# Optimization experiments

Hardware: AMD Instinct MI355X
Metric: run time of the kernel (lower is better)

## Reference

```python
import jax, jax.numpy as jnp
import numpy as np

FEATURE_DIM = 2048
CROP_PE_DIM = 96
FULL = FEATURE_DIM + CROP_PE_DIM  # 2144
H1 = 1024
H2 = 512
NEG_SLOPE = 0.01


def leaky(x):
    return jnp.where(x >= 0, x, NEG_SLOPE * x)


def setup_inputs() -> dict:
    key = jax.random.key(0)
    ks = jax.random.split(key, 8)
    B, T = 512, 32
    features = jax.random.normal(ks[0], (B, T, FULL), dtype=jnp.float32)

    def lin(k, fan_in, fan_out):
        kw, kb = jax.random.split(k)
        bound = 1.0 / np.sqrt(fan_in)
        W = jax.random.uniform(kw, (fan_in, fan_out), minval=-bound, maxval=bound, dtype=jnp.float32)
        b = jax.random.uniform(kb, (fan_out,), minval=-bound, maxval=bound, dtype=jnp.float32)
        return W, b

    We, be = lin(ks[1], 2 * FULL, H1)
    W1a, b1a = lin(ks[2], H1, H1)
    W1b, b1b = lin(ks[3], H1, H2)
    W2a, b2a = lin(ks[4], H2, H2)
    W2b, b2b = lin(ks[5], H2, H2)
    Wd, bd = lin(ks[6], H2, 3)
    return {
        "features": features,
        "We": We, "be": be,
        "W1a": W1a, "b1a": b1a, "W1b": W1b, "b1b": b1b,
        "W2a": W2a, "b2a": b2a, "W2b": W2b, "b2b": b2b,
        "Wd": Wd, "bd": bd,
    }


def reference(features, We, be, W1a, b1a, W1b, b1b, W2a, b2a, W2b, b2b, Wd, bd):
    B, T, D = features.shape
    # Vectorized version of the double Python loop: pair each token with token 0.
    anchor = jnp.broadcast_to(features[:, :1, :], (B, T, D))  # features[i][0]
    features_full = jnp.concatenate((features, anchor), axis=-1).reshape(B * T, 2 * D)
    e_f = features_full @ We + be
    h = leaky(leaky(e_f) @ W1a + b1a)
    h = h @ W1b + b1b  # block1 output
    h2 = leaky(leaky(h) @ W2a + b2a) @ W2b + b2b  # block2
    h = h + h2
    translations = leaky(h) @ Wd + bd  # (B*T, 3)
    bias = jnp.array([[0.0, 0.0, 1.0]], dtype=translations.dtype)
    return translations + bias
```

## Files before the change

### kernel.cpp

```cpp
#include <hip/hip_runtime.h>
#include <hip/hip_bf16.h>
#include <stdint.h>

typedef __attribute__((ext_vector_type(4))) float f32x4;
typedef __attribute__((ext_vector_type(8))) short bf16x8;

#define BK 64

__device__ inline void gload_lds16(const void* g, void* l) {
    __builtin_amdgcn_global_load_lds(
        (const __attribute__((address_space(1))) void*)g,
        (__attribute__((address_space(3))) void*)l, 16, 0, 0);
}

__device__ inline void wg_barrier() {
    asm volatile("s_barrier" ::: "memory");
}
#define SCHED0 __builtin_amdgcn_sched_barrier(0)
#define VMW(n) asm volatile("s_waitcnt vmcnt(" #n ")" ::: "memory")

__device__ inline int xcd_swizzle(int orig, int nwg) {
    int q = nwg >> 3, r = nwg & 7;
    int xcd = orig & 7, idx = orig >> 3;
    int base = (xcd < r) ? xcd * (q + 1) : r * (q + 1) + (xcd - r) * q;
    return base + idx;
}

__device__ inline float b2f(short s) {
    union { float f; unsigned u; } x; x.u = ((unsigned)(unsigned short)s) << 16; return x.f;
}
__device__ inline short f2bs(float f) {
    __hip_bfloat16 h = __float2bfloat16(f);
    short s; __builtin_memcpy(&s, &h, 2); return s;
}

__device__ inline void wt_tile(const float* __restrict__ W, __hip_bfloat16* __restrict__ WT,
                               int K, int N, int KP, int tid, int bid) {
    __shared__ float tile[32][33];
    const int ntn = N >> 5;
    const int tk = bid / ntn, tn = bid - tk * ntn;
    const int k0 = tk * 32, n0 = tn * 32;
    const int c = tid & 31, r8 = tid >> 5;
    #pragma unroll
    for (int p = 0; p < 4; p++) {
        int k = k0 + r8 + p * 8;
        tile[r8 + p * 8][c] = (k < K) ? W[(size_t)k * N + n0 + c] : 0.f;
    }
    __syncthreads();
    #pragma unroll
    for (int p = 0; p < 4; p++) {
        int n = n0 + r8 + p * 8;
        WT[(size_t)n * KP + k0 + c] = __float2bfloat16(tile[c][r8 + p * 8]);
    }
}

__global__ __launch_bounds__(256)
void prepass(const float* __restrict__ feat, __hip_bfloat16* __restrict__ featbf,
             const float* __restrict__ We, __hip_bfloat16* __restrict__ WeTt,
             __hip_bfloat16* __restrict__ WeTb,
             const float* __restrict__ W1a, __hip_bfloat16* __restrict__ W1aT,
             const float* __restrict__ W1b, __hip_bfloat16* __restrict__ W1bT,
             const float* __restrict__ W2a, __hip_bfloat16* __restrict__ W2aT,
             const float* __restrict__ W2b, __hip_bfloat16* __restrict__ W2bT)
{
    const int bid = blockIdx.x;
    const int tid = threadIdx.x;
    if (bid < 17408) {
        int i = bid * 256 + tid;
        int r = i / 272, c8 = (i % 272) * 8;
        __hip_bfloat16 tmp[8];
        if (c8 < 2144) {
            const float4* p = (const float4*)(feat + (size_t)r * 2144 + c8);
            float4 x0 = p[0], x1 = p[1];
            tmp[0] = __float2bfloat16(x0.x); tmp[1] = __float2bfloat16(x0.y);
            tmp[2] = __float2bfloat16(x0.z); tmp[3] = __float2bfloat16(x0.w);
            tmp[4] = __float2bfloat16(x1.x); tmp[5] = __float2bfloat16(x1.y);
            tmp[6] = __float2bfloat16(x1.z); tmp[7] = __float2bfloat16(x1.w);
        } else {
            #pragma unroll
            for (int j = 0; j < 8; j++) tmp[j] = __float2bfloat16(0.f);
        }
        *(bf16x8*)&featbf[(size_t)r * 2176 + c8] = *(const bf16x8*)tmp;
        return;
    }
    int b = bid - 17408;
    if      (b < 2176) wt_tile(We,                WeTt, 2144, 1024, 2176, tid, b);
    else if (b < 4352) wt_tile(We + 2144 * 1024,  WeTb, 2144, 1024, 2176, tid, b - 2176);
    else if (b < 5376) wt_tile(W1a, W1aT, 1024, 1024, 1024, tid, b - 4352);
    else if (b < 5888) wt_tile(W1b, W1bT, 1024,  512, 1024, tid, b - 5376);
    else if (b < 6144) wt_tile(W2a, W2aT,  512,  512,  512, tid, b - 5888);
    else               wt_tile(W2b, W2bT,  512,  512,  512, tid, b - 6144);
}

template<int BN_, int RES_MODE, int OUTK>
__global__ __launch_bounds__(512, 2)
void gemmk(const __hip_bfloat16* __restrict__ A, int lda,
           const __hip_bfloat16* __restrict__ Bt,
           const float* __restrict__ bias,
           const __hip_bfloat16* __restrict__ resb,
           const float* __restrict__ resf,
           __hip_bfloat16* __restrict__ outb,
           __hip_bfloat16* __restrict__ outb2,
           float* __restrict__ outf,
           int M, int N, int K, int gx)
{
    constexpr int NF  = BN_ / 64;
    constexpr int REL = NF * 16;
    __shared__ __hip_bfloat16 lds[2][(256 + BN_) * BK];

    const int nwg  = gridDim.x;
    const int wgid = xcd_swizzle(blockIdx.x, nwg);
    const int by   = wgid / gx;
    const int bx   = wgid - by * gx;

    const int t    = threadIdx.x;
    const int lane = t & 63;
    const int wv   = t >> 6;
    const int wr   = wv >> 2;
    const int wc   = wv & 3;

    const int row0 = by * 256;
    const int col0 = bx * BN_;

    const int NT = K / BK;
    const int split = blockIdx.y;
    const int kb = (split * NT) / gridDim.y;
    const int ke = ((split + 1) * NT) / gridDim.y;
    float* outfs = outf;
    if (OUTK == 0 && gridDim.y > 1) outfs = outf + (size_t)split * M * N;

    const int srow = t >> 3;
    const int sc8  = (t & 7) * 8;
    const int scol = sc8 ^ ((srow & 7) << 3);
    const int sdst = sc8;

    f32x4 acc[8][NF];
    #pragma unroll
    for (int i = 0; i < 8; i++)
        #pragma unroll
        for (int j = 0; j < NF; j++)
            acc[i][j] = f32x4{0.f, 0.f, 0.f, 0.f};

    const int lrow = lane & 15;
    const int lk   = (lane >> 4) * 8;
    const int rxor = (lrow & 7) << 3;

    auto stA = [&](int buf, int k0, int b) {
        gload_lds16(A + (size_t)(row0 + b * 64 + srow) * lda + k0 + scol,
                    &lds[buf][(b * 64 + srow) * BK + sdst]);
    };
    auto stB = [&](int buf, int k0, int b) {
        gload_lds16(Bt + (size_t)(col0 + b * 64 + srow) * K + k0 + scol,
                    &lds[buf][(256 + b * 64 + srow) * BK + sdst]);
    };

    bf16x8 af[4][2];
    auto rdA = [&](int buf, int ih) {
        #pragma unroll
        for (int i = 0; i < 4; ++i)
            #pragma unroll
            for (int h = 0; h < 2; ++h)
                af[i][h] = *(const bf16x8*)
                    &lds[buf][(wr * 128 + (ih * 4 + i) * 16 + lrow) * BK + ((h * 32 + lk) ^ rxor)];
    };
    bf16x8 bgl[2][2], bgh[2][2];
    auto rdB2 = [&](int buf, int jb, bf16x8 (&bg)[2][2]) {
        #pragma unroll
        for (int j = 0; j < 2; ++j)
            #pragma unroll
            for (int h = 0; h < 2; ++h)
                bg[j][h] = *(const bf16x8*)
                    &lds[buf][(256 + wc * REL + (jb + j) * 16 + lrow) * BK + ((h * 32 + lk) ^ rxor)];
    };

#define MFMA_Q(BG, IB, JB)                                                    \
    do {                                                                      \
        __builtin_amdgcn_s_setprio(1);                                        \
        _Pragma("unroll") for (int h_ = 0; h_ < 2; ++h_)                      \
        _Pragma("unroll") for (int i_ = 0; i_ < 4; ++i_)                      \
        _Pragma("unroll") for (int j_ = 0; j_ < 2; ++j_)                      \
            acc[(IB) + i_][(JB) + j_] = __builtin_amdgcn_mfma_f32_16x16x32_bf16( \
                af[i_][h_], BG[j_][h_], acc[(IB) + i_][(JB) + j_], 0, 0, 0);  \
        __builtin_amdgcn_s_setprio(0);                                        \
    } while (0)

    {
        const int k0 = kb * BK, k1 = (kb + 1) * BK;
        if constexpr (NF == 4) {
            stA(0, k0, 0); stA(0, k0, 2); stA(0, k0, 1); stA(0, k0, 3);
            stB(0, k0, 0); stB(0, k0, 1); stB(0, k0, 2); stB(0, k0, 3);
            stA(1, k1, 0); stA(1, k1, 2); stA(1, k1, 1); stA(1, k1, 3);
        } else {
            stA(0, k0, 0); stA(0, k0, 2); stB(0, k0, 0); stB(0, k0, 1);
            stA(0, k0, 1); stA(0, k0, 3);
            stA(1, k1, 0); stA(1, k1, 2); stB(1, k1, 0); stB(1, k1, 1);
        }
    }

    int cur = 0;
    for (int kt = kb; kt < ke; ++kt) {
        const bool pf1 = (kt + 1 < ke), pf2 = (kt + 2 < ke);
        const int nk1 = (kt + 1) * BK, nk2 = (kt + 2) * BK;
        const int nxt = cur ^ 1;
        if constexpr (NF == 4) {
            if (kt == ke - 1) VMW(0); else VMW(4);
            wg_barrier();
            rdA(cur, 0); rdB2(cur, 0, bgl);
            if (pf1) { stB(nxt, nk1, 0); stB(nxt, nk1, 1); }
            SCHED0;
            MFMA_Q(bgl, 0, 0);
            wg_barrier();
            rdB2(cur, 2, bgh);
            if (pf1) { stB(nxt, nk1, 2); stB(nxt, nk1, 3); }
            SCHED0;
            MFMA_Q(bgh, 0, 2);
            wg_barrier();
            rdA(cur, 1);
            if (pf2) { stA(cur, nk2, 0); stA(cur, nk2, 2); }
            SCHED0;
            MFMA_Q(bgl, 4, 0);
            wg_barrier();
            if (pf2) { stA(cur, nk2, 1); stA(cur, nk2, 3); }
            SCHED0;
            MFMA_Q(bgh, 4, 2);
        } else {
            if (kt == ke - 1) VMW(2); else VMW(6);
            wg_barrier();
            rdA(cur, 0); rdB2(cur, 0, bgl);
            if (pf1) { stA(nxt, nk1, 1); stA(nxt, nk1, 3); }
            SCHED0;
            MFMA_Q(bgl, 0, 0);
            if (kt == ke - 1) VMW(0); else VMW(6);
            wg_barrier();
            rdA(cur, 1);
            if (pf2) { stA(cur, nk2, 0); stA(cur, nk2, 2); stB(cur, nk2, 0); stB(cur, nk2, 1); }
            SCHED0;
            MFMA_Q(bgl, 4, 0);
        }
        cur ^= 1;
    }
#undef MFMA_Q

    if constexpr (OUTK == 0) {
        #pragma unroll
        for (int j = 0; j < NF; j++) {
            const int col = col0 + wc * REL + j * 16 + lrow;
            #pragma unroll
            for (int i = 0; i < 8; i++) {
                const int rbase = row0 + wr * 128 + i * 16 + (lane >> 4) * 4;
                #pragma unroll
                for (int r = 0; r < 4; r++)
                    outfs[(size_t)(rbase + r) * N + col] = acc[i][j][r];
            }
        }
    } else {
        wg_barrier();
        __hip_bfloat16* eb = &lds[0][0] + wv * (128 * REL);
        #pragma unroll
        for (int i = 0; i < 8; i++)
            #pragma unroll
            for (int j = 0; j < NF; j++)
                #pragma unroll
                for (int r = 0; r < 4; r++)
                    eb[(i * 16 + (lane >> 4) * 4 + r) * REL + j * 16 + lrow] =
                        __float2bfloat16(acc[i][j][r]);
        constexpr int LPR = REL / 8;
        constexpr int RPI = 64 / LPR;
        constexpr int NIT = 128 / RPI;
        const int lrr = lane / LPR;
        const int lcc = (lane % LPR) * 8;
        const int col = col0 + wc * REL + lcc;
        float bvv[8];
        if (bias) {
            float4 b0 = *(const float4*)&bias[col];
            float4 b1 = *(const float4*)&bias[col + 4];
            bvv[0] = b0.x; bvv[1] = b0.y; bvv[2] = b0.z; bvv[3] = b0.w;
            bvv[4] = b1.x; bvv[5] = b1.y; bvv[6] = b1.z; bvv[7] = b1.w;
        } else {
            #pragma unroll
            for (int e = 0; e < 8; e++) bvv[e] = 0.f;
        }
        #pragma unroll
        for (int it = 0; it < NIT; it++) {
            const int rl  = it * RPI + lrr;
            const int row = row0 + wr * 128 + rl;
            bf16x8 v8 = *(bf16x8*)&eb[rl * REL + lcc];
            float vv[8];
            #pragma unroll
            for (int e = 0; e < 8; e++) vv[e] = b2f(v8[e]) + bvv[e];
            if constexpr (RES_MODE == 1) {
                bf16x8 r8 = *(const bf16x8*)&resb[(size_t)row * N + col];
                #pragma unroll
                for (int e = 0; e < 8; e++) vv[e] += b2f(r8[e]);
            }
            if constexpr (RES_MODE == 2) {
                const float* rp = &resf[(size_t)(row >> 5) * N + col];
                float4 r0 = *(const float4*)rp;
                float4 r1 = *(const float4*)(rp + 4);
                vv[0] += r0.x; vv[1] += r0.y; vv[2] += r0.z; vv[3] += r0.w;
                vv[4] += r1.x; vv[5] += r1.y; vv[6] += r1.z; vv[7] += r1.w;
            }
            bf16x8 o1, o2;
            #pragma unroll
            for (int e = 0; e < 8; e++) {
                float lv = vv[e] >= 0.f ? vv[e] : 0.01f * vv[e];
                if constexpr (OUTK == 1) o1[e] = f2bs(lv);
                if constexpr (OUTK == 2) o1[e] = f2bs(vv[e]);
                if constexpr (OUTK == 3) { o1[e] = f2bs(lv); o2[e] = f2bs(vv[e]); }
            }
            *(bf16x8*)&outb[(size_t)row * N + col] = o1;
            if constexpr (OUTK == 3)
                *(bf16x8*)&outb2[(size_t)row * N + col] = o2;
        }
    }
}

__global__ __launch_bounds__(256)
void anchor_reduce(const float* __restrict__ part, const float* __restrict__ be,
                   float* __restrict__ out) {
    int i = blockIdx.x * 256 + threadIdx.x;
    if (i >= 512 * 1024) return;
    const int S = 512 * 1024;
    int col = i & 1023;
    float s = be[col];
    #pragma unroll
    for (int p = 0; p < 16; p++) s += part[i + p * S];
    out[i] = s;
}

__global__ __launch_bounds__(256)
void final_head(const __hip_bfloat16* __restrict__ h, const float* __restrict__ Wd,
                const float* __restrict__ bd, float* __restrict__ out)
{
    int row  = blockIdx.x * 4 + (threadIdx.x >> 6);
    int lane = threadIdx.x & 63;
    const __hip_bfloat16* hr = h + (size_t)row * 512;
    bf16x8 v8 = *(const bf16x8*)&hr[lane * 8];
    float s0 = 0.f, s1 = 0.f, s2 = 0.f;
    #pragma unroll
    for (int e = 0; e < 8; e++) {
        float v = b2f(v8[e]);
        v = v >= 0.f ? v : 0.01f * v;
        int k = lane * 8 + e;
        s0 += v * Wd[k * 3 + 0];
        s1 += v * Wd[k * 3 + 1];
        s2 += v * Wd[k * 3 + 2];
    }
    #pragma unroll
    for (int off = 32; off > 0; off >>= 1) {
        s0 += __shfl_down(s0, off);
        s1 += __shfl_down(s1, off);
        s2 += __shfl_down(s2, off);
    }
    if (lane == 0) {
        out[row * 3 + 0] = s0 + bd[0];
        out[row * 3 + 1] = s1 + bd[1];
        out[row * 3 + 2] = s2 + bd[2] + 1.0f;
    }
}

extern "C" void kernel_launch(void* const* d_in, const int* in_sizes, int n_in,
                              void* d_out, int out_size, void* d_ws, size_t ws_size,
                              hipStream_t stream)
{
    const float* features = (const float*)d_in[0];
    const float* We  = (const float*)d_in[1];
    const float* be  = (const float*)d_in[2];
    const float* W1a = (const float*)d_in[3];
    const float* b1a = (const float*)d_in[4];
    const float* W1b = (const float*)d_in[5];
    const float* b1b = (const float*)d_in[6];
    const float* W2a = (const float*)d_in[7];
    const float* b2a = (const float*)d_in[8];
    const float* W2b = (const float*)d_in[9];
    const float* b2b = (const float*)d_in[10];
    const float* Wd  = (const float*)d_in[11];
    const float* bd  = (const float*)d_in[12];
    float* out = (float*)d_out;

    char* ws = (char*)d_ws;
    size_t off = 0;
    auto alloc = [&](size_t bytes) -> char* {
        char* p = ws + off;
        off += (bytes + 255) & ~(size_t)255;
        return p;
    };
    __hip_bfloat16* featbf = (__hip_bfloat16*)alloc(16384ull * 2176 * 2);
    __hip_bfloat16* WeTt   = (__hip_bfloat16*)alloc(1024ull * 2176 * 2);
    __hip_bfloat16* WeTb   = (__hip_bfloat16*)alloc(1024ull * 2176 * 2);
    __hip_bfloat16* W1aT   = (__hip_bfloat16*)alloc(1024ull * 1024 * 2);
    __hip_bfloat16* W1bT   = (__hip_bfloat16*)alloc(512ull * 1024 * 2);
    __hip_bfloat16* W2aT   = (__hip_bfloat16*)alloc(512ull * 512 * 2);
    __hip_bfloat16* W2bT   = (__hip_bfloat16*)alloc(512ull * 512 * 2);
    float* eanchor_part    = (float*)alloc(16ull * 512 * 1024 * 4);
    float* eanchor         = (float*)alloc(512ull * 1024 * 4);
    char* bufA             = alloc(16384ull * 1024 * 2);
    char* bufB             = alloc(16384ull * 1024 * 2);
    __hip_bfloat16* h1b    = (__hip_bfloat16*)alloc(16384ull * 512 * 2);

    __hip_bfloat16* act1   = (__hip_bfloat16*)bufA;
    __hip_bfloat16* act2   = (__hip_bfloat16*)bufB;
    __hip_bfloat16* act3   = (__hip_bfloat16*)bufA;
    __hip_bfloat16* act4   = (__hip_bfloat16*)bufB;
    __hip_bfloat16* hsum_b = (__hip_bfloat16*)bufA;

    prepass<<<17408 + 6400, 256, 0, stream>>>(
        features, featbf, We, WeTt, WeTb, W1a, W1aT, W1b, W1bT, W2a, W2aT, W2b, W2bT);

    gemmk<256, 0, 0><<<dim3(8, 16), 512, 0, stream>>>(
        featbf, 32 * 2176, WeTb, nullptr, nullptr, nullptr,
        nullptr, nullptr, eanchor_part, 512, 1024, 2176, 4);
    anchor_reduce<<<2048, 256, 0, stream>>>(eanchor_part, be, eanchor);

    gemmk<256, 2, 1><<<dim3(256), 512, 0, stream>>>(
        featbf, 2176, WeTt, nullptr, nullptr, eanchor,
        act1, nullptr, nullptr, 16384, 1024, 2176, 4);

    gemmk<256, 0, 1><<<dim3(256), 512, 0, stream>>>(
        act1, 1024, W1aT, b1a, nullptr, nullptr,
        act2, nullptr, nullptr, 16384, 1024, 1024, 4);

    gemmk<128, 0, 3><<<dim3(256), 512, 0, stream>>>(
        act2, 1024, W1bT, b1b, nullptr, nullptr,
        act3, h1b, nullptr, 16384, 512, 1024, 4);

    gemmk<128, 0, 1><<<dim3(256), 512, 0, stream>>>(
        act3, 512, W2aT, b2a, nullptr, nullptr,
        act4, nullptr, nullptr, 16384, 512, 512, 4);

    gemmk<128, 1, 2><<<dim3(256), 512, 0, stream>>>(
        act4, 512, W2bT, b2b, h1b, nullptr,
        hsum_b, nullptr, nullptr, 16384, 512, 512, 4);

    final_head<<<4096, 256, 0, stream>>>(hsum_b, Wd, bd, out);
}
```

Measured before the change: 229.6 us.

## Fuse final 512→3 head into last GEMM epilogue, halve anchor split-K

The last GEMM epilogue now applies the leaky activation and the 512x3 head projection in registers, reduces partial sums through shuffles and LDS, and writes per-column-tile partials. A tiny reduce kernel then adds the bias, which removes the bf16 hsum write and its re-read. The prepass feature cast now uses nontemporal loads and stores. The anchor split-K grid drops from 16 to 8 partitions, which means less partial traffic but less parallelism.

```diff
diff --git a/kernel.cpp b/kernel.cpp
--- a/kernel.cpp
+++ b/kernel.cpp
@@ -68,19 +68,18 @@
     if (bid < 17408) {
         int i = bid * 256 + tid;
         int r = i / 272, c8 = (i % 272) * 8;
-        __hip_bfloat16 tmp[8];
+        bf16x8 o;
         if (c8 < 2144) {
-            const float4* p = (const float4*)(feat + (size_t)r * 2144 + c8);
-            float4 x0 = p[0], x1 = p[1];
-            tmp[0] = __float2bfloat16(x0.x); tmp[1] = __float2bfloat16(x0.y);
-            tmp[2] = __float2bfloat16(x0.z); tmp[3] = __float2bfloat16(x0.w);
-            tmp[4] = __float2bfloat16(x1.x); tmp[5] = __float2bfloat16(x1.y);
-            tmp[6] = __float2bfloat16(x1.z); tmp[7] = __float2bfloat16(x1.w);
+            const f32x4* p = (const f32x4*)(feat + (size_t)r * 2144 + c8);
+            f32x4 x0 = __builtin_nontemporal_load(p);
+            f32x4 x1 = __builtin_nontemporal_load(p + 1);
+            o[0] = f2bs(x0[0]); o[1] = f2bs(x0[1]); o[2] = f2bs(x0[2]); o[3] = f2bs(x0[3]);
+            o[4] = f2bs(x1[0]); o[5] = f2bs(x1[1]); o[6] = f2bs(x1[2]); o[7] = f2bs(x1[3]);
         } else {
             #pragma unroll
-            for (int j = 0; j < 8; j++) tmp[j] = __float2bfloat16(0.f);
-        }
-        *(bf16x8*)&featbf[(size_t)r * 2176 + c8] = *(const bf16x8*)tmp;
+            for (int j = 0; j < 8; j++) o[j] = f2bs(0.f);
+        }
+        __builtin_nontemporal_store(o, (bf16x8*)&featbf[(size_t)r * 2176 + c8]);
         return;
     }
     int b = bid - 17408;
@@ -102,6 +101,8 @@
            __hip_bfloat16* __restrict__ outb,
            __hip_bfloat16* __restrict__ outb2,
            float* __restrict__ outf,
+           const float* __restrict__ Wd,
+           float* __restrict__ hpart,
            int M, int N, int K, int gx)
 {
     constexpr int NF  = BN_ / 64;
@@ -256,6 +257,7 @@
     } else {
         wg_barrier();
         __hip_bfloat16* eb = &lds[0][0] + wv * (128 * REL);
+        float* sp = (float*)(&lds[0][0] + 8 * 128 * REL);
         #pragma unroll
         for (int i = 0; i < 8; i++)
             #pragma unroll
@@ -300,17 +302,45 @@
                 vv[0] += r0.x; vv[1] += r0.y; vv[2] += r0.z; vv[3] += r0.w;
                 vv[4] += r1.x; vv[5] += r1.y; vv[6] += r1.z; vv[7] += r1.w;
             }
-            bf16x8 o1, o2;
-            #pragma unroll
-            for (int e = 0; e < 8; e++) {
-                float lv = vv[e] >= 0.f ? vv[e] : 0.01f * vv[e];
-                if constexpr (OUTK == 1) o1[e] = f2bs(lv);
-                if constexpr (OUTK == 2) o1[e] = f2bs(vv[e]);
-                if constexpr (OUTK == 3) { o1[e] = f2bs(lv); o2[e] = f2bs(vv[e]); }
+            if constexpr (OUTK == 4) {
+                float t0 = 0.f, t1 = 0.f, t2 = 0.f;
+                #pragma unroll
+                for (int e = 0; e < 8; e++) {
+                    float lv = vv[e] >= 0.f ? vv[e] : 0.01f * vv[e];
+                    const float* wd = &Wd[(size_t)(col + e) * 3];
+                    t0 += lv * wd[0]; t1 += lv * wd[1]; t2 += lv * wd[2];
+                }
+                t0 += __shfl_xor(t0, 1); t0 += __shfl_xor(t0, 2);
+                t1 += __shfl_xor(t1, 1); t1 += __shfl_xor(t1, 2);
+                t2 += __shfl_xor(t2, 1); t2 += __shfl_xor(t2, 2);
+                if ((lane & 3) == 0) {
+                    float* q = &sp[(size_t)(wr * 128 + rl) * 12 + wc * 3];
+                    q[0] = t0; q[1] = t1; q[2] = t2;
+                }
+            } else {
+                bf16x8 o1, o2;
+                #pragma unroll
+                for (int e = 0; e < 8; e++) {
+                    float lv = vv[e] >= 0.f ? vv[e] : 0.01f * vv[e];
+                    if constexpr (OUTK == 1) o1[e] = f2bs(lv);
+                    if constexpr (OUTK == 2) o1[e] = f2bs(vv[e]);
+                    if constexpr (OUTK == 3) { o1[e] = f2bs(lv); o2[e] = f2bs(vv[e]); }
+                }
+                *(bf16x8*)&outb[(size_t)row * N + col] = o1;
+                if constexpr (OUTK == 3)
+                    *(bf16x8*)&outb2[(size_t)row * N + col] = o2;
             }
-            *(bf16x8*)&outb[(size_t)row * N + col] = o1;
-            if constexpr (OUTK == 3)
-                *(bf16x8*)&outb2[(size_t)row * N + col] = o2;
+        }
+        if constexpr (OUTK == 4) {
+            wg_barrier();
+            if (t < 256) {
+                const float* q = &sp[(size_t)t * 12];
+                float a0 = q[0] + q[3] + q[6] + q[9];
+                float a1 = q[1] + q[4] + q[7] + q[10];
+                float a2 = q[2] + q[5] + q[8] + q[11];
+                float* hp = &hpart[(size_t)(row0 + t) * 12 + bx * 3];
+                hp[0] = a0; hp[1] = a1; hp[2] = a2;
+            }
         }
     }
 }
@@ -324,39 +354,20 @@
     int col = i & 1023;
     float s = be[col];
     #pragma unroll
-    for (int p = 0; p < 16; p++) s += part[i + p * S];
+    for (int p = 0; p < 8; p++) s += part[i + p * S];
     out[i] = s;
 }
 
 __global__ __launch_bounds__(256)
-void final_head(const __hip_bfloat16* __restrict__ h, const float* __restrict__ Wd,
-                const float* __restrict__ bd, float* __restrict__ out)
+void head_reduce(const float* __restrict__ hpart, const float* __restrict__ bd,
+                 float* __restrict__ out)
 {
-    int row  = blockIdx.x * 4 + (threadIdx.x >> 6);
-    int lane = threadIdx.x & 63;
-    const __hip_bfloat16* hr = h + (size_t)row * 512;
-    bf16x8 v8 = *(const bf16x8*)&hr[lane * 8];
-    float s0 = 0.f, s1 = 0.f, s2 = 0.f;
-    #pragma unroll
-    for (int e = 0; e < 8; e++) {
-        float v = b2f(v8[e]);
-        v = v >= 0.f ? v : 0.01f * v;
-        int k = lane * 8 + e;
-        s0 += v * Wd[k * 3 + 0];
-        s1 += v * Wd[k * 3 + 1];
-        s2 += v * Wd[k * 3 + 2];
-    }
-    #pragma unroll
-    for (int off = 32; off > 0; off >>= 1) {
-        s0 += __shfl_down(s0, off);
-        s1 += __shfl_down(s1, off);
-        s2 += __shfl_down(s2, off);
-    }
-    if (lane == 0) {
-        out[row * 3 + 0] = s0 + bd[0];
-        out[row * 3 + 1] = s1 + bd[1];
-        out[row * 3 + 2] = s2 + bd[2] + 1.0f;
-    }
+    int row = blockIdx.x * 256 + threadIdx.x;
+    if (row >= 16384) return;
+    const float* p = hpart + (size_t)row * 12;
+    out[row * 3 + 0] = p[0] + p[3] + p[6] + p[9]  + bd[0];
+    out[row * 3 + 1] = p[1] + p[4] + p[7] + p[10] + bd[1];
+    out[row * 3 + 2] = p[2] + p[5] + p[8] + p[11] + bd[2] + 1.0f;
 }
 
 extern "C" void kernel_launch(void* const* d_in, const int* in_sizes, int n_in,
@@ -392,45 +403,45 @@
     __hip_bfloat16* W1bT   = (__hip_bfloat16*)alloc(512ull * 1024 * 2);
     __hip_bfloat16* W2aT   = (__hip_bfloat16*)alloc(512ull * 512 * 2);
     __hip_bfloat16* W2bT   = (__hip_bfloat16*)alloc(512ull * 512 * 2);
-    float* eanchor_part    = (float*)alloc(16ull * 512 * 1024 * 4);
+    float* eanchor_part    = (float*)alloc(8ull * 512 * 1024 * 4);
     float* eanchor         = (float*)alloc(512ull * 1024 * 4);
     char* bufA             = alloc(16384ull * 1024 * 2);
     char* bufB             = alloc(16384ull * 1024 * 2);
     __hip_bfloat16* h1b    = (__hip_bfloat16*)alloc(16384ull * 512 * 2);
+    float* hpart           = (float*)alloc(16384ull * 12 * 4);
 
     __hip_bfloat16* act1   = (__hip_bfloat16*)bufA;
     __hip_bfloat16* act2   = (__hip_bfloat16*)bufB;
     __hip_bfloat16* act3   = (__hip_bfloat16*)bufA;
     __hip_bfloat16* act4   = (__hip_bfloat16*)bufB;
-    __hip_bfloat16* hsum_b = (__hip_bfloat16*)bufA;
 
     prepass<<<17408 + 6400, 256, 0, stream>>>(
         features, featbf, We, WeTt, WeTb, W1a, W1aT, W1b, W1bT, W2a, W2aT, W2b, W2bT);
 
-    gemmk<256, 0, 0><<<dim3(8, 16), 512, 0, stream>>>(
+    gemmk<256, 0, 0><<<dim3(8, 8), 512, 0, stream>>>(
         featbf, 32 * 2176, WeTb, nullptr, nullptr, nullptr,
-        nullptr, nullptr, eanchor_part, 512, 1024, 2176, 4);
+        nullptr, nullptr, eanchor_part, nullptr, nullptr, 512, 1024, 2176, 4);
     anchor_reduce<<<2048, 256, 0, stream>>>(eanchor_part, be, eanchor);
 
     gemmk<256, 2, 1><<<dim3(256), 512, 0, stream>>>(
         featbf, 2176, WeTt, nullptr, nullptr, eanchor,
-        act1, nullptr, nullptr, 16384, 1024, 2176, 4);
+        act1, nullptr, nullptr, nullptr, nullptr, 16384, 1024, 2176, 4);
 
     gemmk<256, 0, 1><<<dim3(256), 512, 0, stream>>>(
         act1, 1024, W1aT, b1a, nullptr, nullptr,
-        act2, nullptr, nullptr, 16384, 1024, 1024, 4);
+        act2, nullptr, nullptr, nullptr, nullptr, 16384, 1024, 1024, 4);
 
     gemmk<128, 0, 3><<<dim3(256), 512, 0, stream>>>(
         act2, 1024, W1bT, b1b, nullptr, nullptr,
-        act3, h1b, nullptr, 16384, 512, 1024, 4);
+        act3, h1b, nullptr, nullptr, nullptr, 16384, 512, 1024, 4);
 
     gemmk<128, 0, 1><<<dim3(256), 512, 0, stream>>>(
         act3, 512, W2aT, b2a, nullptr, nullptr,
-        act4, nullptr, nullptr, 16384, 512, 512, 4);
-
-    gemmk<128, 1, 2><<<dim3(256), 512, 0, stream>>>(
+        act4, nullptr, nullptr, nullptr, nullptr, 16384, 512, 512, 4);
+
+    gemmk<128, 1, 4><<<dim3(256), 512, 0, stream>>>(
         act4, 512, W2bT, b2b, h1b, nullptr,
-        hsum_b, nullptr, nullptr, 16384, 512, 512, 4);
-
-    final_head<<<4096, 256, 0, stream>>>(hsum_b, Wd, bd, out);
-}
+        nullptr, nullptr, nullptr, Wd, hpart, 16384, 512, 512, 4);
+
+    head_reduce<<<64, 256, 0, stream>>>(hpart, bd, out);
+}
```

After: 221.0 us. 3.7% less time.
